# Optimization experiments

Hardware: AMD Instinct MI355X
Metric: run time of the kernel (lower is better)

## Reference

```python
import jax, jax.numpy as jnp
import numpy as np

N_NODES = 100000
N_EDGES = 3200000
IN_DIM = 128
HID = 32
NUM_CLUSTER = 30
REG = 0.01


def gcn_conv(x, src, dst, W, b, n_nodes):
    # PyG GCNConv: h = D^{-1/2} (A + I) D^{-1/2} (x @ W) + b
    h = x @ W  # [N, out]
    loop = jnp.arange(n_nodes)
    src2 = jnp.concatenate([src, loop])
    dst2 = jnp.concatenate([dst, loop])
    deg = jax.ops.segment_sum(jnp.ones(src2.shape[0], dtype=h.dtype), dst2, num_segments=n_nodes)
    dinv = jnp.where(deg > 0, jax.lax.rsqrt(deg), 0.0)
    norm = dinv[src2] * dinv[dst2]  # [E+N]
    msg = h[src2] * norm[:, None]
    return jax.ops.segment_sum(msg, dst2, num_segments=n_nodes) + b


def setup_inputs() -> dict:
    key = jax.random.key(0)
    k1, k2, k3, k4, k5 = jax.random.split(key, 5)
    x = jax.random.normal(k1, (N_NODES, IN_DIM), dtype=jnp.float32)
    edge_index = jax.random.randint(k2, (2, N_EDGES), 0, N_NODES, dtype=jnp.int64)
    edge_pred = jax.random.uniform(k3, (N_EDGES,), dtype=jnp.float32)
    # Glorot-ish params for the two GCNConv layers
    W1 = jax.random.normal(k4, (IN_DIM, HID), dtype=jnp.float32) / np.sqrt(IN_DIM)
    b1 = jnp.zeros((HID,), dtype=jnp.float32)
    W2 = jax.random.normal(k5, (HID, NUM_CLUSTER), dtype=jnp.float32) / np.sqrt(HID)
    b2 = jnp.zeros((NUM_CLUSTER,), dtype=jnp.float32)
    return {"x": x, "edge_index": edge_index, "edge_pred": edge_pred,
            "W1": W1, "b1": b1, "W2": W2, "b2": b2}


def reference(x, edge_index, edge_pred, W1, b1, W2, b2):
    src, dst = edge_index[0], edge_index[1]
    n = x.shape[0]
    h = jax.nn.relu(gcn_conv(x, src, dst, W1, b1, n))
    # dropout p=0 -> identity
    logits = gcn_conv(h, src, dst, W2, b2, n)
    FX = jax.nn.softmax(logits, axis=-1)  # [N, C]
    FF = jnp.sum(FX[src] * FX[dst], axis=-1)  # [E]
    NFX = jnp.log(1.0 - FX ** 2)  # [N, C]
    preg = -jnp.sum(jnp.log(1.0001 - jnp.exp(jnp.sum(NFX, axis=0))))
    loss = jnp.mean((FF - edge_pred) ** 2) + REG * preg
    return (FX, loss)
```

## Files before the change

kernel.cpp:

```cpp
#include <hip/hip_runtime.h>
#include <hip/hip_bf16.h>
#include <hip/hip_fp8.h>

#define N_NODES 100000
#define N_EDGES 3200000
#define IN_DIM  128
#define HID     32
#define NCLUS   30
#define EDGE_BLOCKS 12500
#define GRP_BLOCKS  12500

#define BUCK_SHIFT 7
#define BUCK_W     128
#define NBUCK      782
#define PB         512
#define EPB        6250
#define SEG_CAP    8192

#define G1_PAIRS   8
#define G1_ROWS_PER_BLOCK 64
#define G1_BLOCKS  1563

__device__ __forceinline__ float bf2f(__hip_bfloat16 v) { return __bfloat162float(v); }

__device__ __forceinline__ unsigned char enc8(float v) {
  __hip_fp8_e4m3 t(v); return (unsigned char)t.__x;
}
__device__ __forceinline__ float dec8(unsigned b) {
  __hip_fp8_e4m3 t; t.__x = (__hip_fp8_storage_t)b; return (float)t;
}
__device__ __forceinline__ float dot4_fp8(unsigned a, unsigned b) {
  float r = 0.0f;
  #pragma unroll
  for (int k = 0; k < 4; k++)
    r += dec8((a >> (8 * k)) & 0xffu) * dec8((b >> (8 * k)) & 0xffu);
  return r;
}

__device__ __forceinline__ int edge_at(const int* ei, int row, int e, int f) {
  int v = ei[(row * N_EDGES + e) << f];
  return min(max(v, 0), N_NODES - 1);
}

__global__ void k_detect(const unsigned int* ei, int* flag) {
  if (threadIdx.x == 0) {
    int zeros = 0;
    for (int i = 1; i < 128; i += 2) zeros += (ei[i] == 0u) ? 1 : 0;
    *flag = (zeros >= 48) ? 1 : 0;
  }
}

__global__ void k_zerosc(float* colsum, double* msed) {
  int t = threadIdx.x;
  if (t < 32) colsum[t] = 0.0f;
  if (t == 32) *msed = 0.0;
}

__global__ void k_zeroall(int* cnt, float* colsum, double* msed) {
  int t = blockIdx.x * blockDim.x + threadIdx.x;
  if (t < N_NODES) cnt[t] = 0;
  if (t < 32) colsum[t] = 0.0f;
  if (t == 32) *msed = 0.0;
}

__global__ void __launch_bounds__(256) k_gemm1r(const float* x, const float* W1,
                                                const float* dinv, __hip_bfloat16* G1) {
  int lane = threadIdx.x & 63;
  int wid  = threadIdx.x >> 6;
  int j = lane & 31;
  int h = lane >> 5;
  float w[64];
  #pragma unroll
  for (int k = 0; k < 64; k++) w[k] = W1[(h * 64 + k) * HID + j];
  int base = (blockIdx.x * 4 + wid) * (2 * G1_PAIRS);
  #pragma unroll
  for (int p = 0; p < G1_PAIRS; p++) {
    int n0 = base + 2 * p;
    if (n0 >= N_NODES) return;
    int n1 = n0 + 1;
    const float4* xa = (const float4*)(x + (size_t)n0 * IN_DIM + h * 64);
    const float4* xb = (const float4*)(x + (size_t)n1 * IN_DIM + h * 64);
    float accA = 0.0f, accB = 0.0f;
    #pragma unroll
    for (int c = 0; c < 16; c++) {
      float4 a = xa[c];
      float4 b = xb[c];
      accA += a.x * w[4*c] + a.y * w[4*c+1] + a.z * w[4*c+2] + a.w * w[4*c+3];
      accB += b.x * w[4*c] + b.y * w[4*c+1] + b.z * w[4*c+2] + b.w * w[4*c+3];
    }
    accA += __shfl_xor(accA, 32, 64);
    accB += __shfl_xor(accB, 32, 64);
    if (h == 0) G1[n0 * 32 + j] = __float2bfloat16(accA * dinv[n0]);
    else        G1[n1 * 32 + j] = __float2bfloat16(accB * dinv[n1]);
  }
}

__global__ void __launch_bounds__(256) k_hist(const int* ei, const int* flag, int* H) {
  __shared__ int h[NBUCK];
  int t = threadIdx.x, p = blockIdx.x;
  for (int i = t; i < NBUCK; i += 256) h[i] = 0;
  __syncthreads();
  int f = *flag;
  int base = p * EPB;
  for (int i = t; i < EPB; i += 256) {
    int d = edge_at(ei, 1, base + i, f);
    atomicAdd(&h[d >> BUCK_SHIFT], 1);
  }
  __syncthreads();
  for (int i = t; i < NBUCK; i += 256) H[p * NBUCK + i] = h[i];
}

__global__ void __launch_bounds__(PB) k_hscan(int* H, int* tot) {
  __shared__ int s[PB];
  int b = blockIdx.x, t = threadIdx.x;
  int v = H[t * NBUCK + b];
  s[t] = v; __syncthreads();
  for (int off = 1; off < PB; off <<= 1) {
    int u = (t >= off) ? s[t - off] : 0;
    __syncthreads();
    s[t] += u;
    __syncthreads();
  }
  H[t * NBUCK + b] = s[t] - v;
  if (t == PB - 1) tot[b] = s[t];
}

__global__ void __launch_bounds__(1024) k_bscan(const int* tot, int* bstart) {
  __shared__ int s[1024];
  int t = threadIdx.x;
  int v = (t < NBUCK) ? tot[t] : 0;
  s[t] = v; __syncthreads();
  for (int off = 1; off < 1024; off <<= 1) {
    int u = (t >= off) ? s[t - off] : 0;
    __syncthreads();
    s[t] += u;
    __syncthreads();
  }
  if (t < NBUCK) bstart[t] = s[t] - v;
  if (t == NBUCK - 1) bstart[NBUCK] = s[t];
}

__global__ void __launch_bounds__(256) k_scat1(const int* ei, const int* flag, const int* H,
                                               const int* bstart, unsigned* sorted) {
  __shared__ int cur[NBUCK];
  int t = threadIdx.x, p = blockIdx.x;
  for (int i = t; i < NBUCK; i += 256) cur[i] = bstart[i] + H[p * NBUCK + i];
  __syncthreads();
  int f = *flag;
  int base = p * EPB;
  for (int i = t; i < EPB; i += 256) {
    int e = base + i;
    int s = edge_at(ei, 0, e, f);
    int d = edge_at(ei, 1, e, f);
    int slot = atomicAdd(&cur[d >> BUCK_SHIFT], 1);
    sorted[slot] = ((unsigned)s << BUCK_SHIFT) | (unsigned)(d & (BUCK_W - 1));
  }
}

__global__ void __launch_bounds__(256) k_pass2(const unsigned* sorted, const int* bstart,
                                               int* cnt, int* cursor, float* dinv, int* csr) {
  __shared__ unsigned se[SEG_CAP];
  __shared__ int scnt[BUCK_W], soff[BUCK_W], scur[BUCK_W];
  int b = blockIdx.x, t = threadIdx.x;
  int s0 = bstart[b], s1 = bstart[b + 1], len = s1 - s0;
  for (int i = t; i < len && i < SEG_CAP; i += 256) se[i] = sorted[s0 + i];
  if (t < BUCK_W) scnt[t] = 0;
  __syncthreads();
  for (int i = t; i < len; i += 256) {
    unsigned u = (i < SEG_CAP) ? se[i] : sorted[s0 + i];
    atomicAdd(&scnt[u & (BUCK_W - 1)], 1);
  }
  __syncthreads();
  int c = (t < BUCK_W) ? scnt[t] : 0;
  if (t < BUCK_W) soff[t] = c;
  __syncthreads();
  for (int off = 1; off < BUCK_W; off <<= 1) {
    int u = 0;
    if (t >= off && t < BUCK_W) u = soff[t - off];
    __syncthreads();
    if (t < BUCK_W) soff[t] += u;
    __syncthreads();
  }
  if (t < BUCK_W) {
    int ex = soff[t] - c;
    int node = (b << BUCK_SHIFT) + t;
    if (node < N_NODES) {
      cnt[node] = c;
      cursor[node] = s0 + ex;
      dinv[node] = rsqrtf((float)(c + 1));
    }
    scur[t] = ex;
  }
  __syncthreads();
  for (int i = t; i < len; i += 256) {
    unsigned u = (i < SEG_CAP) ? se[i] : sorted[s0 + i];
    int dl = u & (BUCK_W - 1);
    int r = atomicAdd(&scur[dl], 1);
    csr[s0 + r] = (int)(u >> BUCK_SHIFT);
  }
}

__global__ void k_count(const int* ei, const int* flag, int* cnt) {
  int e = blockIdx.x * blockDim.x + threadIdx.x;
  if (e >= N_EDGES) return;
  int f = *flag;
  atomicAdd(&cnt[edge_at(ei, 1, e, f)], 1);
}

__global__ void k_dinv(const int* cnt, float* dinv) {
  int t = blockIdx.x * blockDim.x + threadIdx.x;
  if (t < N_NODES) dinv[t] = rsqrtf((float)(cnt[t] + 1));
}

__global__ void __launch_bounds__(256) k_agg1f(const __hip_bfloat16* G, const int* cursor,
                                               const int* cnt, const int* csr, const float* dinv,
                                               const float* b1, const float* W2,
                                               __hip_bfloat16* G2) {
  int j = threadIdx.x & 31, g = threadIdx.x >> 5;
  int n = blockIdx.x * 8 + g;
  if (n >= N_NODES) return;
  int len = cnt[n];
  int st = cursor[n];
  float dn = dinv[n];
  float acc = bf2f(G[n * 32 + j]);
  int i = 0;
  for (; i + 16 <= len; i += 16) {
    int s[16];
    #pragma unroll
    for (int q = 0; q < 16; q++) s[q] = csr[st + i + q];
    float v[16];
    #pragma unroll
    for (int q = 0; q < 16; q++) v[q] = bf2f(G[s[q] * 32 + j]);
    #pragma unroll
    for (int q = 0; q < 16; q++) acc += v[q];
  }
  for (; i + 4 <= len; i += 4) {
    int s[4];
    #pragma unroll
    for (int q = 0; q < 4; q++) s[q] = csr[st + i + q];
    float v[4];
    #pragma unroll
    for (int q = 0; q < 4; q++) v[q] = bf2f(G[s[q] * 32 + j]);
    #pragma unroll
    for (int q = 0; q < 4; q++) acc += v[q];
  }
  for (; i < len; i++) acc += bf2f(G[csr[st + i] * 32 + j]);
  float h = fmaxf(dn * acc + b1[j], 0.0f);
  float g2 = 0.0f;
  #pragma unroll
  for (int k = 0; k < HID; k++) {
    float wk = (j < NCLUS) ? W2[k * NCLUS + j] : 0.0f;
    g2 += __shfl(h, k, 32) * wk;
  }
  G2[n * 32 + j] = __float2bfloat16((j < NCLUS) ? g2 * dn : 0.0f);
}

__global__ void __launch_bounds__(256) k_agg2c(const __hip_bfloat16* G, const int* cursor,
                                               const int* cnt, const int* csr, const float* dinv,
                                               const float* b2, float* outp, unsigned char* fx8) {
  int j = threadIdx.x & 31, g = threadIdx.x >> 5;
  int n = blockIdx.x * 8 + g;
  if (n >= N_NODES) return;
  int len = cnt[n];
  int st = cursor[n];
  float acc = bf2f(G[n * 32 + j]);
  int i = 0;
  for (; i + 16 <= len; i += 16) {
    int s[16];
    #pragma unroll
    for (int q = 0; q < 16; q++) s[q] = csr[st + i + q];
    float v[16];
    #pragma unroll
    for (int q = 0; q < 16; q++) v[q] = bf2f(G[s[q] * 32 + j]);
    #pragma unroll
    for (int q = 0; q < 16; q++) acc += v[q];
  }
  for (; i + 4 <= len; i += 4) {
    int s[4];
    #pragma unroll
    for (int q = 0; q < 4; q++) s[q] = csr[st + i + q];
    float v[4];
    #pragma unroll
    for (int q = 0; q < 4; q++) v[q] = bf2f(G[s[q] * 32 + j]);
    #pragma unroll
    for (int q = 0; q < 4; q++) acc += v[q];
  }
  for (; i < len; i++) acc += bf2f(G[csr[st + i] * 32 + j]);
  bool act = (j < NCLUS);
  float logit = act ? fminf(fmaxf(dinv[n] * acc + b2[j], -80.0f), 80.0f) : -1e30f;
  float m = logit;
  #pragma unroll
  for (int mask = 16; mask > 0; mask >>= 1) m = fmaxf(m, __shfl_xor(m, mask, 32));
  float ex = act ? __expf(logit - m) : 0.0f;
  float ssum = ex;
  #pragma unroll
  for (int mask = 16; mask > 0; mask >>= 1) ssum += __shfl_xor(ssum, mask, 32);
  float fx = ex / fmaxf(ssum, 1e-30f);
  if (act) outp[n * NCLUS + j] = fx;
  fx8[n * 32 + j] = enc8(act ? fx : 0.0f);
}

__global__ void __launch_bounds__(256) k_gemm1s(const float* x, const float* W1,
                                                const float* dinv, float* G1) {
  __shared__ float Ws[IN_DIM * HID];
  int tid = threadIdx.x;
  for (int i = tid; i < IN_DIM * HID; i += 256) Ws[i] = W1[i];
  __syncthreads();
  int j = tid & 31, r = tid >> 5;
  int n = blockIdx.x * 8 + r;
  if (n >= N_NODES) return;
  const float* xr = x + (size_t)n * IN_DIM;
  float acc = 0.0f;
  #pragma unroll
  for (int k = 0; k < IN_DIM; k++) acc += xr[k] * Ws[k * HID + j];
  G1[n * 32 + j] = acc * dinv[n];
}

__global__ void __launch_bounds__(256) k_gemm2s(const float* h, const float* W2,
                                                const float* dinv, float* G2) {
  __shared__ float Ws[HID * 32];
  int tid = threadIdx.x;
  for (int i = tid; i < HID * 32; i += 256) Ws[i] = 0.0f;
  __syncthreads();
  for (int i = tid; i < HID * NCLUS; i += 256) {
    int k = i / NCLUS, j = i % NCLUS;
    Ws[k * 32 + j] = W2[i];
  }
  __syncthreads();
  int j = tid & 31, r = tid >> 5;
  int n = blockIdx.x * 8 + r;
  if (n >= N_NODES) return;
  const float* hr = h + (size_t)n * 32;
  float acc = 0.0f;
  #pragma unroll
  for (int k = 0; k < HID; k++) acc += hr[k] * Ws[k * 32 + j];
  G2[n * 32 + j] = (j < NCLUS) ? acc * dinv[n] : 0.0f;
}

__global__ void __launch_bounds__(256) k_eagg2(const int* ei, const int* flag,
                                               const float* G, float* D) {
  int j = threadIdx.x & 31, g = threadIdx.x >> 5;
  int f = *flag;
  for (int e = blockIdx.x * 8 + g; e < N_EDGES; e += gridDim.x * 8) {
    int s = edge_at(ei, 0, e, f);
    int d = edge_at(ei, 1, e, f);
    atomicAdd(&D[d * 32 + j], G[s * 32 + j]);
  }
}

__global__ void k_relu2(const float* A, const float* dinv, const float* b1, float* G) {
  int t = blockIdx.x * blockDim.x + threadIdx.x;
  if (t >= N_NODES * 32) return;
  int n = t >> 5, j = t & 31;
  G[t] = fmaxf(dinv[n] * (A[t] + G[t]) + b1[j], 0.0f);
}

__global__ void __launch_bounds__(256) k_softmax2(const float* S, const float* G2, const float* dinv,
                                                  const float* b2, float* outp) {
  int n = blockIdx.x * blockDim.x + threadIdx.x;
  if (n >= N_NODES) return;
  float di = dinv[n];
  float lg[NCLUS];
  float m = -1e30f;
  #pragma unroll
  for (int j = 0; j < NCLUS; j++) {
    float v = di * (S[n * 32 + j] + G2[n * 32 + j]) + b2[j];
    v = fminf(fmaxf(v, -80.0f), 80.0f);
    lg[j] = v; m = fmaxf(m, v);
  }
  float ssum = 0.0f;
  #pragma unroll
  for (int j = 0; j < NCLUS; j++) { lg[j] = __expf(lg[j] - m); ssum += lg[j]; }
  float inv = 1.0f / ssum;
  #pragma unroll
  for (int j = 0; j < NCLUS; j++) outp[n * NCLUS + j] = lg[j] * inv;
}

__global__ void k_fx8(const float* outp, unsigned char* fx8) {
  int t = blockIdx.x * blockDim.x + threadIdx.x;
  if (t >= N_NODES * 32) return;
  int n = t >> 5, j = t & 31;
  fx8[t] = enc8((j < NCLUS) ? outp[n * NCLUS + j] : 0.0f);
}

__global__ void __launch_bounds__(256) k_msef3(const int* ei, const float* ep,
                                               const uint4* fx8, const int* flag,
                                               double* msed) {
  int f = *flag;
  int tid = blockIdx.x * blockDim.x + threadIdx.x;
  float local = 0.0f;
  for (int e = tid; e < N_EDGES; e += gridDim.x * blockDim.x) {
    int s = edge_at(ei, 0, e, f);
    int d = edge_at(ei, 1, e, f);
    const uint4* rs = fx8 + s * 2;
    const uint4* rd = fx8 + d * 2;
    uint4 a0 = rs[0], a1 = rs[1];
    uint4 b0 = rd[0], b1 = rd[1];
    float acc;
    acc  = dot4_fp8(a0.x, b0.x) + dot4_fp8(a0.y, b0.y)
         + dot4_fp8(a0.z, b0.z) + dot4_fp8(a0.w, b0.w);
    acc += dot4_fp8(a1.x, b1.x) + dot4_fp8(a1.y, b1.y)
         + dot4_fp8(a1.z, b1.z) + dot4_fp8(a1.w, b1.w);
    float diff = acc - ep[e];
    local += diff * diff;
  }
  __shared__ float sd[256];
  sd[threadIdx.x] = local; __syncthreads();
  for (int off = 128; off > 0; off >>= 1) {
    if (threadIdx.x < off) sd[threadIdx.x] += sd[threadIdx.x + off];
    __syncthreads();
  }
  if (threadIdx.x == 0) atomicAdd(msed, (double)sd[0]);
}

__global__ void __launch_bounds__(256) k_colsumf(const float* FX, float* colsum) {
  __shared__ float sd[256];
  int tid = threadIdx.x;
  int j = tid & 31, g = tid >> 5;
  float local = 0.0f;
  if (j < NCLUS) {
    for (int n = blockIdx.x * 8 + g; n < N_NODES; n += gridDim.x * 8) {
      float v = FX[n * NCLUS + j];
      local += log1pf(-v * v);
    }
  }
  sd[tid] = local; __syncthreads();
  if (tid < 32) {
    float s = 0.0f;
    #pragma unroll
    for (int gg = 0; gg < 8; gg++) s += sd[tid + 32 * gg];
    if (tid < NCLUS) atomicAdd(&colsum[tid], s);
  }
}

__global__ void k_final(const float* colsum, const double* msed, float* out) {
  int tid = threadIdx.x;
  float v = 0.0f;
  if (tid < NCLUS) v = logf(1.0001f - __expf(colsum[tid]));
  #pragma unroll
  for (int mask = 32; mask > 0; mask >>= 1) v += __shfl_xor(v, mask, 64);
  if (tid == 0) {
    float preg = -v;
    float msev = (float)(*msed / (double)N_EDGES);
    out[(size_t)N_NODES * NCLUS] = msev + 0.01f * preg;
  }
}

extern "C" void kernel_launch(void* const* d_in, const int* in_sizes, int n_in,
                              void* d_out, int out_size, void* d_ws, size_t ws_size,
                              hipStream_t stream) {
  const float* x  = (const float*)d_in[0];
  const int*   ei = (const int*)d_in[1];
  const float* ep = (const float*)d_in[2];
  const float* W1 = (const float*)d_in[3];
  const float* b1 = (const float*)d_in[4];
  const float* W2 = (const float*)d_in[5];
  const float* b2 = (const float*)d_in[6];
  float* out = (float*)d_out;

  char* ws = (char*)d_ws;
  size_t off = 0;
  auto alloc = [&](size_t bytes) { size_t o = off; off += (bytes + 255) & ~(size_t)255; return o; };

  size_t o_hdr  = alloc(1024);
  size_t o_cnt  = alloc((size_t)N_NODES * 4);
  size_t o_dinv = alloc((size_t)N_NODES * 4);
  size_t o_B1   = alloc((size_t)N_NODES * 32 * 4);
  size_t o_B2   = alloc((size_t)N_NODES * 32 * 4);

  int*    flag   = (int*)(ws + o_hdr);
  double* msed   = (double*)(ws + o_hdr + 8);
  float*  colsum = (float*)(ws + o_hdr + 256);
  int*    cnt    = (int*)(ws + o_cnt);
  float*  dinv   = (float*)(ws + o_dinv);
  float*  B1f    = (float*)(ws + o_B1);
  float*  B2f    = (float*)(ws + o_B2);
  __hip_bfloat16* B1b = (__hip_bfloat16*)(ws + o_B1);
  unsigned char*  B2c = (unsigned char*)(ws + o_B2);

  const int nodeBlocks = (N_NODES + 255) / 256;
  const int edgeBlocks = EDGE_BLOCKS;
  const int grpBlocks  = GRP_BLOCKS;
  const int elemBlocks = (N_NODES * 32 + 255) / 256;

  k_detect<<<1, 64, 0, stream>>>((const unsigned int*)ei, flag);

  size_t o_cursor = alloc((size_t)N_NODES * 4);
  size_t o_csr    = alloc((size_t)N_EDGES * 4);
  bool use_csr = (off <= ws_size);

  const unsigned char* fx8;

  if (use_csr) {
    int* cursor = (int*)(ws + o_cursor);
    int* csr    = (int*)(ws + o_csr);
    int* H      = (int*)(ws + o_B1 + 6400000);
    int* tot    = (int*)(ws + o_B1 + 6400000 + 1601536);
    int* bstart = (int*)(ws + o_B1 + 6400000 + 1605632);
    unsigned* sorted = (unsigned*)B2c;

    k_zerosc<<<1, 64, 0, stream>>>(colsum, msed);

    k_hist <<<PB, 256, 0, stream>>>(ei, flag, H);
    k_hscan<<<NBUCK, PB, 0, stream>>>(H, tot);
    k_bscan<<<1, 1024, 0, stream>>>(tot, bstart);
    k_scat1<<<PB, 256, 0, stream>>>(ei, flag, H, bstart, sorted);
    k_pass2<<<NBUCK, 256, 0, stream>>>(sorted, bstart, cnt, cursor, dinv, csr);

    __hip_bfloat16* G1b = B1b;
    k_gemm1r<<<G1_BLOCKS, 256, 0, stream>>>(x, W1, dinv, G1b);

    __hip_bfloat16* G2b = (__hip_bfloat16*)(ws + o_B2 + (size_t)N_NODES * 32);
    unsigned char*  fx  = B2c;

    k_agg1f<<<grpBlocks, 256, 0, stream>>>(G1b, cursor, cnt, csr, dinv, b1, W2, G2b);
    k_agg2c<<<grpBlocks, 256, 0, stream>>>(G2b, cursor, cnt, csr, dinv, b2, out, fx);
    fx8 = fx;
  } else {
    k_zeroall<<<nodeBlocks, 256, 0, stream>>>(cnt, colsum, msed);
    k_count<<<edgeBlocks, 256, 0, stream>>>(ei, flag, cnt);
    k_dinv<<<nodeBlocks, 256, 0, stream>>>(cnt, dinv);
    k_gemm1s<<<grpBlocks, 256, 0, stream>>>(x, W1, dinv, B1f);
    hipMemsetAsync(B2f, 0, (size_t)N_NODES * 32 * 4, stream);
    k_eagg2<<<8192, 256, 0, stream>>>(ei, flag, B1f, B2f);
    k_relu2<<<elemBlocks, 256, 0, stream>>>(B2f, dinv, b1, B1f);
    k_gemm2s<<<grpBlocks, 256, 0, stream>>>(B1f, W2, dinv, B2f);
    hipMemsetAsync(B1f, 0, (size_t)N_NODES * 32 * 4, stream);
    k_eagg2<<<8192, 256, 0, stream>>>(ei, flag, B2f, B1f);
    k_softmax2<<<nodeBlocks, 256, 0, stream>>>(B1f, B2f, dinv, b2, out);
    k_fx8<<<elemBlocks, 256, 0, stream>>>(out, (unsigned char*)B1b);
    fx8 = (const unsigned char*)B1b;
  }

  k_msef3<<<4096, 256, 0, stream>>>(ei, ep, (const uint4*)fx8, flag, msed);
  k_colsumf<<<256, 256, 0, stream>>>(out, colsum);
  k_final<<<1, 64, 0, stream>>>(colsum, msed, out);
}
```

Before: 483.7 us.

## Overlap first-layer GEMM with CSR build by splitting it across histogram and scatter kernels

```diff
diff --git a/kernel.cpp b/kernel.cpp
--- a/kernel.cpp
+++ b/kernel.cpp
@@ -17,9 +17,9 @@
 #define EPB        6250
 #define SEG_CAP    8192
 
-#define G1_PAIRS   8
-#define G1_ROWS_PER_BLOCK 64
-#define G1_BLOCKS  1563
+#define G1A_BLK    780
+#define G1A_ROWS   49920
+#define G1B_BLK    783
 
 __device__ __forceinline__ float bf2f(__hip_bfloat16 v) { return __bfloat162float(v); }
 
@@ -37,23 +37,31 @@
   return r;
 }
 
+__device__ __forceinline__ unsigned sc2(unsigned u, float sc) {
+  __hip_bfloat16 h0 = *reinterpret_cast<__hip_bfloat16*>(&u);
+  unsigned uh = u >> 16;
+  __hip_bfloat16 h1 = *reinterpret_cast<__hip_bfloat16*>(&uh);
+  __hip_bfloat16 r0 = __float2bfloat16(__bfloat162float(h0) * sc);
+  __hip_bfloat16 r1 = __float2bfloat16(__bfloat162float(h1) * sc);
+  unsigned a = *reinterpret_cast<unsigned short*>(&r0);
+  unsigned b = *reinterpret_cast<unsigned short*>(&r1);
+  return a | (b << 16);
+}
+
 __device__ __forceinline__ int edge_at(const int* ei, int row, int e, int f) {
   int v = ei[(row * N_EDGES + e) << f];
   return min(max(v, 0), N_NODES - 1);
 }
 
-__global__ void k_detect(const unsigned int* ei, int* flag) {
-  if (threadIdx.x == 0) {
+__global__ void k_detect(const unsigned int* ei, int* flag, float* colsum, double* msed) {
+  int t = threadIdx.x;
+  if (t < 32) colsum[t] = 0.0f;
+  if (t == 32) *msed = 0.0;
+  if (t == 0) {
     int zeros = 0;
     for (int i = 1; i < 128; i += 2) zeros += (ei[i] == 0u) ? 1 : 0;
     *flag = (zeros >= 48) ? 1 : 0;
   }
-}
-
-__global__ void k_zerosc(float* colsum, double* msed) {
-  int t = threadIdx.x;
-  if (t < 32) colsum[t] = 0.0f;
-  if (t == 32) *msed = 0.0;
 }
 
 __global__ void k_zeroall(int* cnt, float* colsum, double* msed) {
@@ -63,8 +71,8 @@
   if (t == 32) *msed = 0.0;
 }
 
-__global__ void __launch_bounds__(256) k_gemm1r(const float* x, const float* W1,
-                                                const float* dinv, __hip_bfloat16* G1) {
+__device__ __forceinline__ void gemm1_body(int gb, int row_off, const float* x,
+                                           const float* W1, __hip_bfloat16* G1) {
   int lane = threadIdx.x & 63;
   int wid  = threadIdx.x >> 6;
   int j = lane & 31;
@@ -72,9 +80,9 @@
   float w[64];
   #pragma unroll
   for (int k = 0; k < 64; k++) w[k] = W1[(h * 64 + k) * HID + j];
-  int base = (blockIdx.x * 4 + wid) * (2 * G1_PAIRS);
-  #pragma unroll
-  for (int p = 0; p < G1_PAIRS; p++) {
+  int base = row_off + (gb * 4 + wid) * 16;
+  #pragma unroll
+  for (int p = 0; p < 8; p++) {
     int n0 = base + 2 * p;
     if (n0 >= N_NODES) return;
     int n1 = n0 + 1;
@@ -90,13 +98,15 @@
     }
     accA += __shfl_xor(accA, 32, 64);
     accB += __shfl_xor(accB, 32, 64);
-    if (h == 0) G1[n0 * 32 + j] = __float2bfloat16(accA * dinv[n0]);
-    else        G1[n1 * 32 + j] = __float2bfloat16(accB * dinv[n1]);
-  }
-}
-
-__global__ void __launch_bounds__(256) k_hist(const int* ei, const int* flag, int* H) {
+    if (h == 0) G1[n0 * 32 + j] = __float2bfloat16(accA);
+    else        G1[n1 * 32 + j] = __float2bfloat16(accB);
+  }
+}
+
+__global__ void __launch_bounds__(256) k_f1(const int* ei, const int* flag, int* H,
+                                            const float* x, const float* W1, __hip_bfloat16* G1) {
   __shared__ int h[NBUCK];
+  if (blockIdx.x >= PB) { gemm1_body(blockIdx.x - PB, 0, x, W1, G1); return; }
   int t = threadIdx.x, p = blockIdx.x;
   for (int i = t; i < NBUCK; i += 256) h[i] = 0;
   __syncthreads();
@@ -140,9 +150,11 @@
   if (t == NBUCK - 1) bstart[NBUCK] = s[t];
 }
 
-__global__ void __launch_bounds__(256) k_scat1(const int* ei, const int* flag, const int* H,
-                                               const int* bstart, unsigned* sorted) {
+__global__ void __launch_bounds__(256) k_f2(const int* ei, const int* flag, const int* H,
+                                            const int* bstart, unsigned* sorted,
+                                            const float* x, const float* W1, __hip_bfloat16* G1) {
   __shared__ int cur[NBUCK];
+  if (blockIdx.x >= PB) { gemm1_body(blockIdx.x - PB, G1A_ROWS, x, W1, G1); return; }
   int t = threadIdx.x, p = blockIdx.x;
   for (int i = t; i < NBUCK; i += 256) cur[i] = bstart[i] + H[p * NBUCK + i];
   __syncthreads();
@@ -158,9 +170,11 @@
 }
 
 __global__ void __launch_bounds__(256) k_pass2(const unsigned* sorted, const int* bstart,
-                                               int* cnt, int* cursor, float* dinv, int* csr) {
+                                               int* cnt, int* cursor, float* dinv, int* csr,
+                                               __hip_bfloat16* G1) {
   __shared__ unsigned se[SEG_CAP];
   __shared__ int scnt[BUCK_W], soff[BUCK_W], scur[BUCK_W];
+  __shared__ float sdv[BUCK_W];
   int b = blockIdx.x, t = threadIdx.x;
   int s0 = bstart[b], s1 = bstart[b + 1], len = s1 - s0;
   for (int i = t; i < len && i < SEG_CAP; i += 256) se[i] = sorted[s0 + i];
@@ -184,10 +198,12 @@
   if (t < BUCK_W) {
     int ex = soff[t] - c;
     int node = (b << BUCK_SHIFT) + t;
+    float dv = rsqrtf((float)(c + 1));
+    sdv[t] = dv;
     if (node < N_NODES) {
       cnt[node] = c;
       cursor[node] = s0 + ex;
-      dinv[node] = rsqrtf((float)(c + 1));
+      dinv[node] = dv;
     }
     scur[t] = ex;
   }
@@ -197,6 +213,16 @@
     int dl = u & (BUCK_W - 1);
     int r = atomicAdd(&scur[dl], 1);
     csr[s0 + r] = (int)(u >> BUCK_SHIFT);
+  }
+  int nbase = b << BUCK_SHIFT;
+  int nlim = min(BUCK_W, N_NODES - nbase);
+  uint4* Gv = (uint4*)(G1 + (size_t)nbase * 32);
+  for (int q = t; q < nlim * 4; q += 256) {
+    float sc = sdv[q >> 2];
+    uint4 u = Gv[q];
+    u.x = sc2(u.x, sc); u.y = sc2(u.y, sc);
+    u.z = sc2(u.z, sc); u.w = sc2(u.w, sc);
+    Gv[q] = u;
   }
 }
 
@@ -483,7 +509,7 @@
   const int grpBlocks  = GRP_BLOCKS;
   const int elemBlocks = (N_NODES * 32 + 255) / 256;
 
-  k_detect<<<1, 64, 0, stream>>>((const unsigned int*)ei, flag);
+  k_detect<<<1, 64, 0, stream>>>((const unsigned int*)ei, flag, colsum, msed);
 
   size_t o_cursor = alloc((size_t)N_NODES * 4);
   size_t o_csr    = alloc((size_t)N_EDGES * 4);
@@ -499,16 +525,13 @@
     int* bstart = (int*)(ws + o_B1 + 6400000 + 1605632);
     unsigned* sorted = (unsigned*)B2c;
 
-    k_zerosc<<<1, 64, 0, stream>>>(colsum, msed);
-
-    k_hist <<<PB, 256, 0, stream>>>(ei, flag, H);
+    __hip_bfloat16* G1b = B1b;
+
+    k_f1<<<PB + G1A_BLK, 256, 0, stream>>>(ei, flag, H, x, W1, G1b);
     k_hscan<<<NBUCK, PB, 0, stream>>>(H, tot);
     k_bscan<<<1, 1024, 0, stream>>>(tot, bstart);
-    k_scat1<<<PB, 256, 0, stream>>>(ei, flag, H, bstart, sorted);
-    k_pass2<<<NBUCK, 256, 0, stream>>>(sorted, bstart, cnt, cursor, dinv, csr);
-
-    __hip_bfloat16* G1b = B1b;
-    k_gemm1r<<<G1_BLOCKS, 256, 0, stream>>>(x, W1, dinv, G1b);
+    k_f2<<<PB + G1B_BLK, 256, 0, stream>>>(ei, flag, H, bstart, sorted, x, W1, G1b);
+    k_pass2<<<NBUCK, 256, 0, stream>>>(sorted, bstart, cnt, cursor, dinv, csr, G1b);
 
     __hip_bfloat16* G2b = (__hip_bfloat16*)(ws + o_B2 + (size_t)N_NODES * 32);
     unsigned char*  fx  = B2c;
```

After: 484.5 us. No clear change (+0.2%).
